# Optimization experiments

Hardware: AMD Instinct MI355X
Metric: run time of the kernel (lower is better)

## Reference

```python
import jax, jax.numpy as jnp
import numpy as np

V, E, H = 32000, 50, 100
B, T = 8, 512


def setup_inputs() -> dict:
    key = jax.random.key(0)
    ks = jax.random.split(key, 12)
    inputs = jax.random.randint(ks[0], (B, T), 0, V, dtype=jnp.int64)
    d = {
        "inputs": inputs,
        "embedding": jax.random.normal(ks[1], (V, E), jnp.float32),
        "W_hr": jax.random.normal(ks[2], (H, H), jnp.float32) * 0.01,
        "W_xr": jax.random.normal(ks[3], (E, H), jnp.float32) * 0.01,
        "b_r": jnp.zeros((H,), jnp.float32),
        "W_hz": jax.random.normal(ks[4], (H, H), jnp.float32) * 0.01,
        "W_xz": jax.random.normal(ks[5], (E, H), jnp.float32) * 0.01,
        "b_z": jnp.zeros((H,), jnp.float32),
        "W_hh": jax.random.normal(ks[6], (H, H), jnp.float32) * 0.01,
        "W_xh": jax.random.normal(ks[7], (E, H), jnp.float32) * 0.01,
        "b_h": jnp.zeros((H,), jnp.float32),
        "fc_W": jax.random.normal(ks[8], (H, V), jnp.float32) * 0.01,
        "fc_b": jnp.zeros((V,), jnp.float32),
    }
    return d


def reference(inputs, embedding, W_hr, W_xr, b_r, W_hz, W_xz, b_z,
              W_hh, W_xh, b_h, fc_W, fc_b):
    # Embed all timesteps at once: [B, T, E] -> time-major [T, B, E]
    x = embedding[inputs]
    x_tm = jnp.transpose(x, (1, 0, 2))

    h0 = jnp.zeros((inputs.shape[0], W_hr.shape[0]), dtype=embedding.dtype)

    def step(h_t, x_t):
        R_t = jax.nn.sigmoid(h_t @ W_hr + x_t @ W_xr + b_r)
        Z_t = jax.nn.sigmoid(h_t @ W_hz + x_t @ W_xz + b_z)
        # NOTE: original torch code computes (R_t * h_t) @ W_hh (left-to-right precedence)
        h_tilda = jnp.tanh((R_t * h_t) @ W_hh + x_t @ W_xh + b_h)
        h_new = Z_t * h_tilda + (1.0 - Z_t) * h_t
        y_t = h_new @ fc_W + fc_b  # [B, V]
        return h_new, y_t

    _, ys = jax.lax.scan(step, h0, x_tm)  # ys: [T, B, V]
    return jnp.transpose(ys, (1, 0, 2))   # [B, T, V]
```

## Files before the change

kernel.cpp:

```cpp
#include <hip/hip_runtime.h>
#include <hip/hip_bf16.h>
#include <hip/hip_fp16.h>
#include <math.h>

#define NV 32000
#define NE 50
#define NH 100
#define NB 8
#define NT 512
#define KP 112
#define HS 136

#define NBLK   256
#define NCONS  (NBLK - NB)
#define NMT    (NT * NB / 32)
#define NNT    (NV / 256)
#define NTILE  (NMT * NNT)

typedef __attribute__((ext_vector_type(8)))  _Float16 f16x8;
typedef __attribute__((ext_vector_type(4)))  float    f32x4;
typedef __attribute__((ext_vector_type(16))) float    f32x16;

__device__ __forceinline__ void bar_lgkm() {
    __builtin_amdgcn_sched_barrier(0);
    asm volatile("s_waitcnt lgkmcnt(0)" ::: "memory");
    __builtin_amdgcn_s_barrier();
    asm volatile("" ::: "memory");
    __builtin_amdgcn_sched_barrier(0);
}

__device__ __forceinline__ void store_hp(_Float16* p, float v) {
    _Float16 h = (_Float16)v;
    unsigned short u = __builtin_bit_cast(unsigned short, h);
    __hip_atomic_store((unsigned short*)p, u, __ATOMIC_RELAXED,
                       __HIP_MEMORY_SCOPE_AGENT);
}

__global__ void init_kernel(int* __restrict__ ctr)
{
    if (threadIdx.x < NB)
        __hip_atomic_store(ctr + threadIdx.x, 0, __ATOMIC_RELAXED,
                           __HIP_MEMORY_SCOPE_AGENT);
}

__global__ __launch_bounds__(256) void convw_kernel(
    const float* __restrict__ W, _Float16* __restrict__ Wp)
{
    int wv = threadIdx.x >> 6, l = threadIdx.x & 63;
    int ct = blockIdx.x * 4 + wv;
    int v  = ct * 32 + (l & 31);
    int kb = (l >> 5) * 8;
    _Float16* dst = Wp + (size_t)ct * 7 * 512 + l * 8;
    for (int kt = 0; kt < 7; kt++) {
        f16x8 tmp;
        #pragma unroll
        for (int j = 0; j < 8; j++) {
            int k = kt * 16 + kb + j;
            tmp[j] = (_Float16)(k < NH ? W[(size_t)k * NV + v] : 0.0f);
        }
        *(f16x8*)(dst + (size_t)kt * 512) = tmp;
    }
}

__global__ __launch_bounds__(64) void convg_kernel(
    const float* __restrict__ Whr, const float* __restrict__ Whz,
    const float* __restrict__ Whh, _Float16* __restrict__ Wg)
{
    int f = blockIdx.x;
    int g = f / 28, rem = f % 28, n = rem / 4, kt = rem % 4;
    const float* W = (g == 0) ? Whr : (g == 1) ? Whz : Whh;
    int l   = threadIdx.x;
    int col = n * 16 + (l & 15);
    int k0  = kt * 32 + (l >> 4) * 8;
    f16x8 v;
    #pragma unroll
    for (int j = 0; j < 8; j++) {
        int k = k0 + j;
        v[j] = (_Float16)((k < NH && col < NH) ? W[k * NH + col] : 0.0f);
    }
    *(f16x8*)(Wg + (size_t)f * 512 + l * 8) = v;
}

__global__ __launch_bounds__(128) void xproj_kernel(
    const int* __restrict__ inp, const float* __restrict__ emb,
    const float* __restrict__ Wxr, const float* __restrict__ br,
    const float* __restrict__ Wxz, const float* __restrict__ bz,
    const float* __restrict__ Wxh, const float* __restrict__ bh,
    float* __restrict__ Xr, float* __restrict__ Xz, float* __restrict__ Xh)
{
    int n = blockIdx.x;
    int t = n >> 3, b = n & 7;
    __shared__ float xs[NE];
    int tid = threadIdx.x;
    int idx = inp[b * NT + t];
    if (tid < NE) xs[tid] = emb[idx * NE + tid];
    __syncthreads();
    if (tid < NH) {
        float ar = br[tid], az = bz[tid], ah = bh[tid];
        for (int e = 0; e < NE; e++) {
            float x = xs[e];
            ar += x * Wxr[e * NH + tid];
            az += x * Wxz[e * NH + tid];
            ah += x * Wxh[e * NH + tid];
        }
        Xr[n * NH + tid] = ar;
        Xz[n * NH + tid] = az;
        Xh[n * NH + tid] = ah;
    }
}

__global__ __launch_bounds__(256) void fused_kernel(
    const _Float16* __restrict__ Wg,
    const float* __restrict__ Xr, const float* __restrict__ Xz,
    const float* __restrict__ Xh, _Float16* __restrict__ Hp,
    const _Float16* __restrict__ Wp, const float* __restrict__ fcb,
    float* __restrict__ out, int* __restrict__ ctr)
{
    __shared__ __align__(16) _Float16 h16[16 * HS];
    __shared__ __align__(16) _Float16 rh16[16 * HS];

    int tid = threadIdx.x;

    if (blockIdx.x < NB) {
        __builtin_amdgcn_s_setprio(1);
        int b   = blockIdx.x;
        int w   = tid >> 6, l = tid & 63;
        int lj  = l & 15;

        for (int i = tid; i < 16 * HS; i += 256) { h16[i] = (_Float16)0.0f; rh16[i] = (_Float16)0.0f; }
        __syncthreads();

        int n0 = w, n1 = w + 4;
        bool has1 = (n1 < 7);
        int n1c = has1 ? n1 : n0;

        f16x8 WR0[4], WZ0[4], WH0[4], WR1[4], WZ1[4], WH1[4];
        #pragma unroll
        for (int kt = 0; kt < 4; kt++) {
            WR0[kt] = *(const f16x8*)(Wg + (size_t)(((0*7 + n0)*4 + kt))*512 + l*8);
            WZ0[kt] = *(const f16x8*)(Wg + (size_t)(((1*7 + n0)*4 + kt))*512 + l*8);
            WH0[kt] = *(const f16x8*)(Wg + (size_t)(((2*7 + n0)*4 + kt))*512 + l*8);
            WR1[kt] = *(const f16x8*)(Wg + (size_t)(((0*7 + n1c)*4 + kt))*512 + l*8);
            WZ1[kt] = *(const f16x8*)(Wg + (size_t)(((1*7 + n1c)*4 + kt))*512 + l*8);
            WH1[kt] = *(const f16x8*)(Wg + (size_t)(((2*7 + n1c)*4 + kt))*512 + l*8);
        }

        int j0 = n0 * 16 + lj;
        int j1 = n1c * 16 + lj;
        int j0x = j0 < NH ? j0 : NH - 1;
        int j1x = j1 < NH ? j1 : NH - 1;

        float h0 = 0.0f, h1 = 0.0f;
        float xr0, xz0, xh0, xr1, xz1, xh1;
        if (l < 16) {
            int base = b * NH;
            xr0 = Xr[base + j0x]; xz0 = Xz[base + j0x]; xh0 = Xh[base + j0x];
            xr1 = Xr[base + j1x]; xz1 = Xz[base + j1x]; xh1 = Xh[base + j1x];
        }

        int aoff = lj * HS + (l >> 4) * 8;

        for (int t = 0; t < NT; t++) {
            float pr0, pz0, ph0, pr1, pz1, ph1;
            if (l < 16 && t + 1 < NT) {
                int base = ((t + 1) * NB + b) * NH;
                pr0 = Xr[base + j0x]; pz0 = Xz[base + j0x]; ph0 = Xh[base + j0x];
                pr1 = Xr[base + j1x]; pz1 = Xz[base + j1x]; ph1 = Xh[base + j1x];
            }

            f32x4 aR0 = {0,0,0,0}, aZ0 = {0,0,0,0}, aR1 = {0,0,0,0}, aZ1 = {0,0,0,0};
            #pragma unroll
            for (int kt = 0; kt < 4; kt++) {
                f16x8 a = *(const f16x8*)&h16[aoff + kt * 32];
                aR0 = __builtin_amdgcn_mfma_f32_16x16x32_f16(a, WR0[kt], aR0, 0, 0, 0);
                aZ0 = __builtin_amdgcn_mfma_f32_16x16x32_f16(a, WZ0[kt], aZ0, 0, 0, 0);
                aR1 = __builtin_amdgcn_mfma_f32_16x16x32_f16(a, WR1[kt], aR1, 0, 0, 0);
                aZ1 = __builtin_amdgcn_mfma_f32_16x16x32_f16(a, WZ1[kt], aZ1, 0, 0, 0);
            }
            float z0 = 0.0f, z1 = 0.0f;
            if (l < 16) {
                float r0 = 1.0f / (1.0f + __expf(-(aR0[0] + xr0)));
                z0       = 1.0f / (1.0f + __expf(-(aZ0[0] + xz0)));
                rh16[j0] = (_Float16)(j0 < NH ? r0 * h0 : 0.0f);
                if (has1) {
                    float r1 = 1.0f / (1.0f + __expf(-(aR1[0] + xr1)));
                    z1       = 1.0f / (1.0f + __expf(-(aZ1[0] + xz1)));
                    rh16[j1] = (_Float16)(j1 < NH ? r1 * h1 : 0.0f);
                }
            }
            bar_lgkm();

            f32x4 aH0 = {0,0,0,0}, aH1 = {0,0,0,0};
            #pragma unroll
            for (int kt = 0; kt < 4; kt++) {
                f16x8 a = *(const f16x8*)&rh16[aoff + kt * 32];
                aH0 = __builtin_amdgcn_mfma_f32_16x16x32_f16(a, WH0[kt], aH0, 0, 0, 0);
                aH1 = __builtin_amdgcn_mfma_f32_16x16x32_f16(a, WH1[kt], aH1, 0, 0, 0);
            }
            if (l < 16) {
                size_t hpb = (size_t)(t * NB + b) * KP;
                {
                    float e  = __expf(2.0f * (aH0[0] + xh0));
                    float ht = 1.0f - 2.0f / (e + 1.0f);
                    float hn = fmaf(z0, ht - h0, h0);
                    hn = (j0 < NH) ? hn : 0.0f;
                    h0 = hn;
                    h16[j0] = (_Float16)hn;
                    store_hp(Hp + hpb + j0, hn);
                }
                if (has1) {
                    float e  = __expf(2.0f * (aH1[0] + xh1));
                    float ht = 1.0f - 2.0f / (e + 1.0f);
                    float hn = fmaf(z1, ht - h1, h1);
                    hn = (j1 < NH) ? hn : 0.0f;
                    h1 = hn;
                    h16[j1] = (_Float16)hn;
                    store_hp(Hp + hpb + j1, hn);
                }
            }
            bar_lgkm();

            if ((t & 7) == 7) {
                asm volatile("s_waitcnt vmcnt(0)" ::: "memory");
                __syncthreads();
                if (tid == 0)
                    __hip_atomic_store(ctr + b, t + 1, __ATOMIC_RELAXED,
                                       __HIP_MEMORY_SCOPE_AGENT);
            }

            xr0 = pr0; xz0 = pz0; xh0 = ph0;
            xr1 = pr1; xz1 = pz1; xh1 = ph1;
        }
    } else {
        int wv = tid >> 6, l = tid & 63;
        int done_upto = 0;

        for (int tile = (int)blockIdx.x - NB; tile < NTILE; tile += NCONS) {
            int mt  = tile / NNT;
            int ntl = tile - mt * NNT;
            int need = mt * 4 + 4;

            if (need > done_upto) {
                if (tid == 0) {
                    #pragma unroll 1
                    for (int bi = 0; bi < NB; ++bi)
                        while (__hip_atomic_load(ctr + bi, __ATOMIC_RELAXED,
                                                 __HIP_MEMORY_SCOPE_AGENT) < need)
                            __builtin_amdgcn_s_sleep(8);
                }
                __syncthreads();
                done_upto = need;
            }

            int n0 = mt * 32;
            int cb = ntl * 256 + wv * 64;

            const _Float16* arow = Hp + (size_t)(n0 + (l & 31)) * KP + (l >> 5) * 8;
            f16x8 a[7];
            #pragma unroll
            for (int kt = 0; kt < 7; kt++)
                a[kt] = *(const f16x8*)(arow + kt * 16);

            int ct0 = cb >> 5;
            const _Float16* bp = Wp + (size_t)ct0 * 7 * 512 + l * 8;

            f32x16 acc0 = {0,0,0,0,0,0,0,0,0,0,0,0,0,0,0,0};
            f32x16 acc1 = {0,0,0,0,0,0,0,0,0,0,0,0,0,0,0,0};
            #pragma unroll
            for (int kt = 0; kt < 7; kt++) {
                f16x8 b0 = *(const f16x8*)(bp + (size_t)kt * 512);
                f16x8 b1 = *(const f16x8*)(bp + (size_t)(kt + 7) * 512);
                acc0 = __builtin_amdgcn_mfma_f32_32x32x16_f16(a[kt], b0, acc0, 0, 0, 0);
                acc1 = __builtin_amdgcn_mfma_f32_32x32x16_f16(a[kt], b1, acc1, 0, 0, 0);
            }

            int c0 = cb + (l & 31);
            float bias0 = fcb[c0], bias1 = fcb[c0 + 32];
            #pragma unroll
            for (int p = 0; p < 16; p++) {
                int r = (p & 3) + 8 * (p >> 2) + 4 * (l >> 5);
                int m = n0 + r;
                size_t row = (size_t)(m & 7) * NT + (m >> 3);
                out[row * NV + c0]      = acc0[p] + bias0;
                out[row * NV + c0 + 32] = acc1[p] + bias1;
            }
        }
    }
}

extern "C" void kernel_launch(void* const* d_in, const int* in_sizes, int n_in,
                              void* d_out, int out_size, void* d_ws, size_t ws_size,
                              hipStream_t stream)
{
    const int*   inp = (const int*)  d_in[0];
    const float* emb = (const float*)d_in[1];
    const float* Whr = (const float*)d_in[2];
    const float* Wxr = (const float*)d_in[3];
    const float* br  = (const float*)d_in[4];
    const float* Whz = (const float*)d_in[5];
    const float* Wxz = (const float*)d_in[6];
    const float* bz  = (const float*)d_in[7];
    const float* Whh = (const float*)d_in[8];
    const float* Wxh = (const float*)d_in[9];
    const float* bh  = (const float*)d_in[10];
    const float* fcW = (const float*)d_in[11];
    const float* fcb = (const float*)d_in[12];
    float* out = (float*)d_out;

    float*    Xr = (float*)d_ws;
    float*    Xz = Xr + NT * NB * NH;
    float*    Xh = Xz + NT * NB * NH;
    _Float16* Hp = (_Float16*)(Xh + NT * NB * NH);
    _Float16* Wp = Hp + (size_t)NT * NB * KP;
    _Float16* Wg = Wp + (size_t)1000 * 7 * 512;
    int*      ct = (int*)(Wg + (size_t)84 * 512);

    init_kernel<<<1, 64, 0, stream>>>(ct);
    convw_kernel<<<NV / 32 / 4, 256, 0, stream>>>(fcW, Wp);
    convg_kernel<<<84, 64, 0, stream>>>(Whr, Whz, Whh, Wg);
    xproj_kernel<<<NT * NB, 128, 0, stream>>>(inp, emb, Wxr, br, Wxz, bz, Wxh, bh,
                                              Xr, Xz, Xh);
    fused_kernel<<<NBLK, 256, 0, stream>>>(Wg, Xr, Xz, Xh, Hp, Wp, fcb, out, ct);
}
```

Measured before the change: 652.6 us.

## Pin consumer blocks to fixed column tiles and keep FC weights in registers

```diff
diff --git a/kernel.cpp b/kernel.cpp
--- a/kernel.cpp
+++ b/kernel.cpp
@@ -15,7 +15,6 @@
 #define NCONS  (NBLK - NB)
 #define NMT    (NT * NB / 32)
 #define NNT    (NV / 256)
-#define NTILE  (NMT * NNT)
 
 typedef __attribute__((ext_vector_type(8)))  _Float16 f16x8;
 typedef __attribute__((ext_vector_type(4)))  float    f32x4;
@@ -232,50 +231,58 @@
             xr1 = pr1; xz1 = pz1; xh1 = ph1;
         }
     } else {
+        int c  = (int)blockIdx.x - NB;
         int wv = tid >> 6, l = tid & 63;
+        int ntl, mlo, mhi;
+        if (c < NNT) { ntl = c;       mlo = 0;       mhi = (ntl < NNT - 2) ? NMT / 2 : NMT; }
+        else         { ntl = c - NNT; mlo = NMT / 2; mhi = NMT; }
+
+        int cb  = ntl * 256 + wv * 64;
+        int ct0 = cb >> 5;
+        const _Float16* bp = Wp + (size_t)ct0 * 7 * 512 + l * 8;
+        f16x8 wb0[7], wb1[7];
+        #pragma unroll
+        for (int kt = 0; kt < 7; kt++) {
+            wb0[kt] = *(const f16x8*)(bp + (size_t)kt * 512);
+            wb1[kt] = *(const f16x8*)(bp + (size_t)(kt + 7) * 512);
+        }
+        int c0 = cb + (l & 31);
+        float bias0 = fcb[c0], bias1 = fcb[c0 + 32];
+
         int done_upto = 0;
-
-        for (int tile = (int)blockIdx.x - NB; tile < NTILE; tile += NCONS) {
-            int mt  = tile / NNT;
-            int ntl = tile - mt * NNT;
+        for (int mt = mlo; mt < mhi; mt++) {
             int need = mt * 4 + 4;
-
             if (need > done_upto) {
                 if (tid == 0) {
                     #pragma unroll 1
-                    for (int bi = 0; bi < NB; ++bi)
-                        while (__hip_atomic_load(ctr + bi, __ATOMIC_RELAXED,
-                                                 __HIP_MEMORY_SCOPE_AGENT) < need)
-                            __builtin_amdgcn_s_sleep(8);
+                    for (int bi = 0; bi < NB; ++bi) {
+                        int cur;
+                        while ((cur = __hip_atomic_load(ctr + bi, __ATOMIC_RELAXED,
+                                                        __HIP_MEMORY_SCOPE_AGENT)) < need) {
+                            if (need - cur > 16) __builtin_amdgcn_s_sleep(64);
+                            else                 __builtin_amdgcn_s_sleep(8);
+                        }
+                    }
                 }
                 __syncthreads();
                 done_upto = need;
             }
 
             int n0 = mt * 32;
-            int cb = ntl * 256 + wv * 64;
-
             const _Float16* arow = Hp + (size_t)(n0 + (l & 31)) * KP + (l >> 5) * 8;
             f16x8 a[7];
             #pragma unroll
             for (int kt = 0; kt < 7; kt++)
                 a[kt] = *(const f16x8*)(arow + kt * 16);
 
-            int ct0 = cb >> 5;
-            const _Float16* bp = Wp + (size_t)ct0 * 7 * 512 + l * 8;
-
             f32x16 acc0 = {0,0,0,0,0,0,0,0,0,0,0,0,0,0,0,0};
             f32x16 acc1 = {0,0,0,0,0,0,0,0,0,0,0,0,0,0,0,0};
             #pragma unroll
             for (int kt = 0; kt < 7; kt++) {
-                f16x8 b0 = *(const f16x8*)(bp + (size_t)kt * 512);
-                f16x8 b1 = *(const f16x8*)(bp + (size_t)(kt + 7) * 512);
-                acc0 = __builtin_amdgcn_mfma_f32_32x32x16_f16(a[kt], b0, acc0, 0, 0, 0);
-                acc1 = __builtin_amdgcn_mfma_f32_32x32x16_f16(a[kt], b1, acc1, 0, 0, 0);
-            }
-
-            int c0 = cb + (l & 31);
-            float bias0 = fcb[c0], bias1 = fcb[c0 + 32];
+                acc0 = __builtin_amdgcn_mfma_f32_32x32x16_f16(a[kt], wb0[kt], acc0, 0, 0, 0);
+                acc1 = __builtin_amdgcn_mfma_f32_32x32x16_f16(a[kt], wb1[kt], acc1, 0, 0, 0);
+            }
+
             #pragma unroll
             for (int p = 0; p < 16; p++) {
                 int r = (p & 3) + 8 * (p >> 2) + 4 * (l >> 5);
```

New measurement: 634.1 us. -2.8%, faster.
